# Kernel optimization log

Hardware: AMD Instinct MI355X
Metric: run time of the kernel (lower is better)

The kernel has to match this reference:

```python
import jax, jax.numpy as jnp
import numpy as np

# db4 (Daubechies-4) lowpass decomposition filter, L = 8 taps
DB4 = np.array([0.23037781330885523, 0.7148465705525415, 0.6308807679295904,
                -0.027983769416983849, -0.18703481171888114, 0.030841381835986965,
                0.032883011666982945, -0.010597401784997278], dtype=np.float32)


def setup_inputs() -> dict:
    key = jax.random.key(0)
    x = jax.random.normal(key, (4, 256, 256, 256), dtype=jnp.float32)
    h = jnp.asarray(DB4)
    return {"x": x, "h": h}


def _corr_valid(u, f):
    # u: [..., T], f: [L]; cross-correlation with VALID padding (== tf.nn.conv1d)
    L = f.shape[0]
    B = int(np.prod(u.shape[:-1]))
    out = jax.lax.conv_general_dilated(
        u.reshape(B, 1, u.shape[-1]), f.reshape(1, 1, L),
        window_strides=(1,), padding='VALID',
        dimension_numbers=('NCW', 'OIW', 'NCW'))
    return out.reshape(u.shape[:-1] + (out.shape[-1],))


def _recon_axis(s, w, h0, h1, axis):
    # s, w: scale / wavelet coefficient halves, same shape; recon along `axis`
    L = h0.shape[0]
    P = (L - 2) // 2 + 1  # number of periodic-wrap samples (= L//2 for even L)
    x = jnp.stack([s, w])                      # [2, ...]
    x = jnp.moveaxis(x, axis + 1, -1)          # bring recon axis to last
    N = x.shape[-1]
    # periodic extension (cyclic gather of last P) then drop first -> len N+P-1
    x = jnp.concatenate([x[..., N - P:], x], axis=-1)[..., 1:]
    # zero-interleaved upsample: [0, x0, 0, x1, ...], then one trailing zero -> len 2N+L-1
    up = jnp.stack([jnp.zeros_like(x), x], axis=-1).reshape(x.shape[:-1] + (-1,))
    up = jnp.pad(up, [(0, 0)] * (up.ndim - 1) + [(0, 1)])
    y = _corr_valid(up[0], h0) + _corr_valid(up[1], h1)  # [..., 2N]
    return jnp.moveaxis(y, -1, axis)


def reference(x, h):
    h0 = h[::-1]                                        # reversed lowpass
    sign = jnp.where(jnp.arange(h.shape[0]) % 2 == 0, -1.0, 1.0).astype(h.dtype)
    h1 = sign * h                                       # QMF highpass (double reverse cancels)
    out = x
    for axis in range(1, x.ndim):
        s, w = jnp.split(out, 2, axis=axis)
        out = _recon_axis(s, w, h0, h1, axis)
    return out
```

## Files before the change

kernel.cpp:

```cpp
#include <hip/hip_runtime.h>


#define FILT_DECL(h)                                          \
  const float a0 = h[6], a1 = h[4], a2 = h[2], a3 = h[0];     \
  const float b0 = h[7], b1 = h[5], b2 = h[3], b3 = h[1];     \
  const float c0 = h[1], c1 = h[3], c2 = h[5], c3 = h[7];     \
  const float d0 = -h[0], d1 = -h[2], d2 = -h[4], d3 = -h[6];

#define Y0(s0,s1,s2,s3,w0,w1,w2,w3)                                        \
  fmaf(w3, c3, fmaf(w2, c2, fmaf(w1, c1, fmaf(w0, c0,                      \
  fmaf(s3, a3, fmaf(s2, a2, fmaf(s1, a1, s0 * a0)))))))
#define Y1(s0,s1,s2,s3,w0,w1,w2,w3)                                        \
  fmaf(w3, d3, fmaf(w2, d2, fmaf(w1, d1, fmaf(w0, d0,                      \
  fmaf(s3, b3, fmaf(s2, b2, fmaf(s1, b1, s0 * b0)))))))

__global__ __launch_bounds__(256) void wav_axis1_s(const float* __restrict__ in,
                                                   float* __restrict__ tmp,
                                                   const float* __restrict__ h) {
  const int inner = blockIdx.x * 256 + threadIdx.x;
  const int m0 = blockIdx.y * 64;
  const size_t base = (size_t)blockIdx.z * (256u * 65536u) + (unsigned)inner;
  const float* __restrict__ ps = in + base;
  const float* __restrict__ pw = in + base + (size_t)128 * 65536;
  float* __restrict__ po = tmp + base;
  FILT_DECL(h)
  float s0 = __builtin_nontemporal_load(&ps[(size_t)((m0 - 3) & 127) * 65536]);
  float s1 = __builtin_nontemporal_load(&ps[(size_t)((m0 - 2) & 127) * 65536]);
  float s2 = __builtin_nontemporal_load(&ps[(size_t)((m0 - 1) & 127) * 65536]);
  float w0 = __builtin_nontemporal_load(&pw[(size_t)((m0 - 3) & 127) * 65536]);
  float w1 = __builtin_nontemporal_load(&pw[(size_t)((m0 - 2) & 127) * 65536]);
  float w2 = __builtin_nontemporal_load(&pw[(size_t)((m0 - 1) & 127) * 65536]);
  for (int m = m0; m < m0 + 64; ++m) {
    const float s3 = __builtin_nontemporal_load(&ps[(size_t)m * 65536]);
    const float w3 = __builtin_nontemporal_load(&pw[(size_t)m * 65536]);
    po[(size_t)(2 * m) * 65536] = Y0(s0, s1, s2, s3, w0, w1, w2, w3);
    po[(size_t)(2 * m + 1) * 65536] = Y1(s0, s1, s2, s3, w0, w1, w2, w3);
    s0 = s1; s1 = s2; s2 = s3;
    w0 = w1; w1 = w2; w2 = w3;
  }
}

#define LSTR 260
__global__ __launch_bounds__(512, 8) void wav_t23w(const float* __restrict__ tmp,
                                                   float* __restrict__ out,
                                                   const float* __restrict__ hg) {
  __shared__ __align__(16) float lb[38 * LSTR];
  const int t = threadIdx.x;
  const int d2t = blockIdx.x;
  const size_t slice = blockIdx.y;
  const float* __restrict__ src = tmp + slice * 65536;
  FILT_DECL(hg)
  const int mb2 = 16 * d2t - 3;

#pragma unroll
  for (int k = 0; k < 4; ++k) {
    const int e = t + 512 * k;
    const int i2 = e >> 6, q4 = e & 63;
    const int g2 = (i2 < 19) ? ((mb2 + i2) & 127) : (128 + ((mb2 + i2 - 19) & 127));
    *reinterpret_cast<float4*>(&lb[i2 * LSTR + 4 * q4]) =
        *reinterpret_cast<const float4*>(src + (g2 << 8) + 4 * q4);
  }
  if (t < 384) {
    const int e = t + 2048;
    const int i2 = e >> 6, q4 = e & 63;
    const int g2 = (i2 < 19) ? ((mb2 + i2) & 127) : (128 + ((mb2 + i2 - 19) & 127));
    *reinterpret_cast<float4*>(&lb[i2 * LSTR + 4 * q4]) =
        *reinterpret_cast<const float4*>(src + (g2 << 8) + 4 * q4);
  }
  __syncthreads();

  {
    const int j = t >> 1, p0 = (t & 1) * 8;
    float S[11], W[11];
#pragma unroll
    for (int i = 0; i < 11; ++i) S[i] = lb[(p0 + i) * LSTR + j];
#pragma unroll
    for (int i = 0; i < 11; ++i) W[i] = lb[(19 + p0 + i) * LSTR + j];
    asm volatile("" ::: "memory");
#pragma unroll
    for (int q = 0; q < 8; ++q) {
      const int p = p0 + q;
      lb[p * LSTR + j]        = Y0(S[q], S[q+1], S[q+2], S[q+3], W[q], W[q+1], W[q+2], W[q+3]);
      lb[(19 + p) * LSTR + j] = Y1(S[q], S[q+1], S[q+2], S[q+3], W[q], W[q+1], W[q+2], W[q+3]);
    }
  }
  __syncthreads();

  const int r = t >> 4, m0 = (t & 15) * 8;
  const int prow = ((r & 1) ? (19 + (r >> 1)) : (r >> 1)) * LSTR;
  float S[11], W[11];
#pragma unroll
  for (int i = 0; i < 11; ++i) {
    const int cs = (m0 + i - 3) & 127;
    S[i] = lb[prow + cs];
    W[i] = lb[prow + 128 + cs];
  }
  float* __restrict__ dst = out + slice * 65536
      + (size_t)(32 * d2t + r) * 256 + 16 * (t & 15);
#pragma unroll
  for (int g = 0; g < 4; ++g) {
    float4 y;
    y.x = Y0(S[2*g],   S[2*g+1], S[2*g+2], S[2*g+3], W[2*g],   W[2*g+1], W[2*g+2], W[2*g+3]);
    y.y = Y1(S[2*g],   S[2*g+1], S[2*g+2], S[2*g+3], W[2*g],   W[2*g+1], W[2*g+2], W[2*g+3]);
    y.z = Y0(S[2*g+1], S[2*g+2], S[2*g+3], S[2*g+4], W[2*g+1], W[2*g+2], W[2*g+3], W[2*g+4]);
    y.w = Y1(S[2*g+1], S[2*g+2], S[2*g+3], S[2*g+4], W[2*g+1], W[2*g+2], W[2*g+3], W[2*g+4]);
    *reinterpret_cast<float4*>(dst + 4 * g) = y;
  }
}

__global__ __launch_bounds__(256) void wav_axis1(const float* __restrict__ in,
                                                 float* __restrict__ out,
                                                 const float* __restrict__ h) {
  const int inner = blockIdx.x * 256 + threadIdx.x;
  const int m0 = blockIdx.y * 64;
  const size_t base = (size_t)blockIdx.z * (256u * 65536u) + (unsigned)inner;
  const float* __restrict__ ps = in + base;
  const float* __restrict__ pw = in + base + (size_t)128 * 65536;
  float* __restrict__ po = out + base;
  FILT_DECL(h)
  float s0 = ps[(size_t)((m0 - 3) & 127) * 65536];
  float s1 = ps[(size_t)((m0 - 2) & 127) * 65536];
  float s2 = ps[(size_t)((m0 - 1) & 127) * 65536];
  float w0 = pw[(size_t)((m0 - 3) & 127) * 65536];
  float w1 = pw[(size_t)((m0 - 2) & 127) * 65536];
  float w2 = pw[(size_t)((m0 - 1) & 127) * 65536];
  for (int m = m0; m < m0 + 64; ++m) {
    const float s3 = ps[(size_t)m * 65536];
    const float w3 = pw[(size_t)m * 65536];
    po[(size_t)(2 * m) * 65536] = Y0(s0, s1, s2, s3, w0, w1, w2, w3);
    po[(size_t)(2 * m + 1) * 65536] = Y1(s0, s1, s2, s3, w0, w1, w2, w3);
    s0 = s1; s1 = s2; s2 = s3;
    w0 = w1; w1 = w2; w2 = w3;
  }
}

__global__ __launch_bounds__(256) void wav_axis2(float* __restrict__ buf,
                                                 const float* __restrict__ h) {
  __shared__ float tile[256][32];
  const int t = threadIdx.x;
  const int c = t & 31;
  const int g = t >> 5;
  const size_t slice = (size_t)(blockIdx.x >> 3);
  const int col0 = (blockIdx.x & 7) * 32;
  float* __restrict__ p = buf + slice * 65536 + col0;
#pragma unroll
  for (int i = 0; i < 32; ++i) {
    const int rr = i * 8 + g;
    tile[rr][c] = p[rr * 256 + c];
  }
  __syncthreads();
  FILT_DECL(h)
  const int m0 = g * 16;
  float s0 = tile[(m0 - 3) & 127][c];
  float s1 = tile[(m0 - 2) & 127][c];
  float s2 = tile[(m0 - 1) & 127][c];
  float w0 = tile[128 + ((m0 - 3) & 127)][c];
  float w1 = tile[128 + ((m0 - 2) & 127)][c];
  float w2 = tile[128 + ((m0 - 1) & 127)][c];
#pragma unroll
  for (int m = m0; m < m0 + 16; ++m) {
    const float s3 = tile[m][c];
    const float w3 = tile[128 + m][c];
    p[(2 * m) * 256 + c] = Y0(s0, s1, s2, s3, w0, w1, w2, w3);
    p[(2 * m + 1) * 256 + c] = Y1(s0, s1, s2, s3, w0, w1, w2, w3);
    s0 = s1; s1 = s2; s2 = s3;
    w0 = w1; w1 = w2; w2 = w3;
  }
}

__global__ __launch_bounds__(256) void wav_axis3(float* __restrict__ buf,
                                                 const float* __restrict__ h) {
  __shared__ float tile[512];
  const int t = threadIdx.x;
  float* __restrict__ p = buf + (size_t)blockIdx.x * 512;
  tile[t] = p[t];
  tile[256 + t] = p[256 + t];
  __syncthreads();
  FILT_DECL(h)
  const int rr = t >> 7;
  const int m = t & 127;
  const float* __restrict__ line = tile + rr * 256;
  const float s0 = line[(m - 3) & 127];
  const float s1 = line[(m - 2) & 127];
  const float s2 = line[(m - 1) & 127];
  const float s3 = line[m];
  const float w0 = line[128 + ((m - 3) & 127)];
  const float w1 = line[128 + ((m - 2) & 127)];
  const float w2 = line[128 + ((m - 1) & 127)];
  const float w3 = line[128 + m];
  float2 y;
  y.x = Y0(s0, s1, s2, s3, w0, w1, w2, w3);
  y.y = Y1(s0, s1, s2, s3, w0, w1, w2, w3);
  *reinterpret_cast<float2*>(p + rr * 256 + 2 * m) = y;
}

extern "C" void kernel_launch(void* const* d_in, const int* in_sizes, int n_in,
                              void* d_out, int out_size, void* d_ws, size_t ws_size,
                              hipStream_t stream) {
  const float* x = (const float*)d_in[0];
  const float* h = (const float*)d_in[1];
  float* out = (float*)d_out;
  const size_t need = (size_t)4 * 256 * 256 * 256 * 4;

  if (ws_size >= need) {
    float* tmp = (float*)d_ws;
    wav_axis1_s<<<dim3(256, 2, 4), 256, 0, stream>>>(x, tmp, h);
    wav_t23w<<<dim3(8, 1024), 512, 0, stream>>>(tmp, out, h);
  } else {
    wav_axis1<<<dim3(256, 2, 4), 256, 0, stream>>>(x, out, h);
    wav_axis2<<<dim3(8192), 256, 0, stream>>>(out, h);
    wav_axis3<<<dim3(131072), 256, 0, stream>>>(out, h);
  }
}
```

Baseline: 233.8 us.

## Load tile via direct global-to-LDS loads and add periodic halo columns

The fused axis-2/3 kernel now fills shared memory with global_load_lds dword loads, which bypass registers, in place of float4 loads staged through registers. The LDS layout gains three-element periodic halo columns for each half, written during the axis-2 pass, and the row stride changes to 264. This lets the axis-3 pass read its 11-element windows with vectorized float4/float2 LDS reads instead of wrapped scalar indexing. The cost is 19 scalar 4-byte async loads per thread instead of about 4.75 float4 loads, plus extra divergent halo stores.

```diff
diff --git a/kernel.cpp b/kernel.cpp
--- a/kernel.cpp
+++ b/kernel.cpp
@@ -13,6 +13,14 @@
 #define Y1(s0,s1,s2,s3,w0,w1,w2,w3)                                        \
   fmaf(w3, d3, fmaf(w2, d2, fmaf(w1, d1, fmaf(w0, d0,                      \
   fmaf(s3, b3, fmaf(s2, b2, fmaf(s1, b1, s0 * b0)))))))
+
+__device__ __forceinline__ void gload_lds4(const float* g, float* l) {
+  auto gp = reinterpret_cast<const __attribute__((address_space(1))) int*>(
+      reinterpret_cast<uintptr_t>(g));
+  auto lp = reinterpret_cast<__attribute__((address_space(3))) int*>(
+      reinterpret_cast<uintptr_t>(l));
+  __builtin_amdgcn_global_load_lds(gp, lp, 4, 0, 0);
+}
 
 __global__ __launch_bounds__(256) void wav_axis1_s(const float* __restrict__ in,
                                                    float* __restrict__ tmp,
@@ -40,8 +48,8 @@
   }
 }
 
-#define LSTR 260
-__global__ __launch_bounds__(512, 8) void wav_t23w(const float* __restrict__ tmp,
+#define LSTR 264
+__global__ __launch_bounds__(512, 8) void wav_t23h(const float* __restrict__ tmp,
                                                    float* __restrict__ out,
                                                    const float* __restrict__ hg) {
   __shared__ __align__(16) float lb[38 * LSTR];
@@ -53,35 +61,37 @@
   const int mb2 = 16 * d2t - 3;
 
 #pragma unroll
-  for (int k = 0; k < 4; ++k) {
+  for (int k = 0; k < 19; ++k) {
     const int e = t + 512 * k;
-    const int i2 = e >> 6, q4 = e & 63;
+    const int i2 = e >> 8, c = e & 255;
     const int g2 = (i2 < 19) ? ((mb2 + i2) & 127) : (128 + ((mb2 + i2 - 19) & 127));
-    *reinterpret_cast<float4*>(&lb[i2 * LSTR + 4 * q4]) =
-        *reinterpret_cast<const float4*>(src + (g2 << 8) + 4 * q4);
-  }
-  if (t < 384) {
-    const int e = t + 2048;
-    const int i2 = e >> 6, q4 = e & 63;
-    const int g2 = (i2 < 19) ? ((mb2 + i2) & 127) : (128 + ((mb2 + i2 - 19) & 127));
-    *reinterpret_cast<float4*>(&lb[i2 * LSTR + 4 * q4]) =
-        *reinterpret_cast<const float4*>(src + (g2 << 8) + 4 * q4);
+    const int phys = c + ((c < 128) ? 3 : 7);
+    gload_lds4(src + (g2 << 8) + c, &lb[i2 * LSTR + phys]);
   }
   __syncthreads();
 
   {
     const int j = t >> 1, p0 = (t & 1) * 8;
+    const int pj = j + ((j < 128) ? 3 : 7);
     float S[11], W[11];
 #pragma unroll
-    for (int i = 0; i < 11; ++i) S[i] = lb[(p0 + i) * LSTR + j];
-#pragma unroll
-    for (int i = 0; i < 11; ++i) W[i] = lb[(19 + p0 + i) * LSTR + j];
+    for (int i = 0; i < 11; ++i) S[i] = lb[(p0 + i) * LSTR + pj];
+#pragma unroll
+    for (int i = 0; i < 11; ++i) W[i] = lb[(19 + p0 + i) * LSTR + pj];
     asm volatile("" ::: "memory");
+    const int hcol = (j >= 125 && j < 128) ? (j - 125)
+                   : ((j >= 253) ? (j - 121) : -1);
 #pragma unroll
     for (int q = 0; q < 8; ++q) {
       const int p = p0 + q;
-      lb[p * LSTR + j]        = Y0(S[q], S[q+1], S[q+2], S[q+3], W[q], W[q+1], W[q+2], W[q+3]);
-      lb[(19 + p) * LSTR + j] = Y1(S[q], S[q+1], S[q+2], S[q+3], W[q], W[q+1], W[q+2], W[q+3]);
+      const float y0 = Y0(S[q], S[q+1], S[q+2], S[q+3], W[q], W[q+1], W[q+2], W[q+3]);
+      const float y1 = Y1(S[q], S[q+1], S[q+2], S[q+3], W[q], W[q+1], W[q+2], W[q+3]);
+      lb[p * LSTR + pj] = y0;
+      lb[(19 + p) * LSTR + pj] = y1;
+      if (hcol >= 0) {
+        lb[p * LSTR + hcol] = y0;
+        lb[(19 + p) * LSTR + hcol] = y1;
+      }
     }
   }
   __syncthreads();
@@ -89,11 +99,19 @@
   const int r = t >> 4, m0 = (t & 15) * 8;
   const int prow = ((r & 1) ? (19 + (r >> 1)) : (r >> 1)) * LSTR;
   float S[11], W[11];
-#pragma unroll
-  for (int i = 0; i < 11; ++i) {
-    const int cs = (m0 + i - 3) & 127;
-    S[i] = lb[prow + cs];
-    W[i] = lb[prow + 128 + cs];
+  {
+    const float4 sa = *reinterpret_cast<const float4*>(&lb[prow + m0]);
+    const float4 sb = *reinterpret_cast<const float4*>(&lb[prow + m0 + 4]);
+    const float2 sc = *reinterpret_cast<const float2*>(&lb[prow + m0 + 8]);
+    S[0]=sa.x; S[1]=sa.y; S[2]=sa.z; S[3]=sa.w;
+    S[4]=sb.x; S[5]=sb.y; S[6]=sb.z; S[7]=sb.w;
+    S[8]=sc.x; S[9]=sc.y; S[10]=lb[prow + m0 + 10];
+    const float4 wa = *reinterpret_cast<const float4*>(&lb[prow + 132 + m0]);
+    const float4 wb = *reinterpret_cast<const float4*>(&lb[prow + 132 + m0 + 4]);
+    const float2 wc = *reinterpret_cast<const float2*>(&lb[prow + 132 + m0 + 8]);
+    W[0]=wa.x; W[1]=wa.y; W[2]=wa.z; W[3]=wa.w;
+    W[4]=wb.x; W[5]=wb.y; W[6]=wb.z; W[7]=wb.w;
+    W[8]=wc.x; W[9]=wc.y; W[10]=lb[prow + 132 + m0 + 10];
   }
   float* __restrict__ dst = out + slice * 65536
       + (size_t)(32 * d2t + r) * 256 + 16 * (t & 15);
@@ -205,7 +223,7 @@
   if (ws_size >= need) {
     float* tmp = (float*)d_ws;
     wav_axis1_s<<<dim3(256, 2, 4), 256, 0, stream>>>(x, tmp, h);
-    wav_t23w<<<dim3(8, 1024), 512, 0, stream>>>(tmp, out, h);
+    wav_t23h<<<dim3(8, 1024), 512, 0, stream>>>(tmp, out, h);
   } else {
     wav_axis1<<<dim3(256, 2, 4), 256, 0, stream>>>(x, out, h);
     wav_axis2<<<dim3(8192), 256, 0, stream>>>(out, h);
```

New measurement: 223.3 us. 1.05x faster.
